# Optimization experiments

Hardware: AMD Instinct MI355X
Metric: run time of the kernel (lower is better)

The kernel has to match this reference:

```python
import jax, jax.numpy as jnp
import numpy as np

B, N, D_IN, D_OUT, R = 8, 2048, 256, 256, 4


def setup_inputs() -> dict:
    key = jax.random.key(0)
    k1, k2, k3, k4 = jax.random.split(key, 4)
    x = jax.random.normal(k1, (B, N, D_IN), dtype=jnp.float32)
    adj = jnp.zeros((1,), dtype=jnp.float32)  # unused by the module
    # relation-type matrix: 0 = no edge, 1..R = relation id
    relation = jax.random.randint(k2, (B, N, N), 0, R + 1, dtype=jnp.int32)
    weight = jax.random.normal(k3, (R, D_IN, D_OUT), dtype=jnp.float32) * 0.05
    bias = jax.random.normal(k4, (D_OUT,), dtype=jnp.float32) * 0.05
    return {"x": x, "adj": adj, "relation": relation, "weight": weight, "bias": bias}


def reference(x, adj, relation, weight, bias):
    # Binary per-relation adjacency masks: [R, B, N, N]
    rel_ids = jnp.arange(1, weight.shape[0] + 1, dtype=relation.dtype)
    masks = (relation[None] == rel_ids[:, None, None, None]).astype(x.dtype)
    # Aggregate neighbors per relation: h[r] = A_r @ x  -> [R, B, N, D_in]
    h = jnp.einsum('rbnm,bmd->rbnd', masks, x)
    # Per-relation output transform, summed over relations: [B, N, D_out]
    y = jnp.einsum('rbnd,rdo->bno', h, weight)
    return y + bias
```

## Files before the change

kernel.cpp:

```cpp
#include <hip/hip_runtime.h>
#include <hip/hip_bf16.h>
#include <stdint.h>

typedef uint32_t u32;
typedef uint64_t u64;
typedef __bf16 bf16x8 __attribute__((ext_vector_type(8)));
typedef float f32x4 __attribute__((ext_vector_type(4)));
typedef u32 u32x4 __attribute__((ext_vector_type(4)));

#define NB 8
#define NN 2048
#define DIN 256
#define DOUT 256
#define NR 4
#define KTOT (NN * NR)

#define XW_BYTES   (NB * DOUT * KTOT * 2)
#define PART_BYTES (NB * NN * DOUT * 4)

__device__ __forceinline__ ushort f2bf(float f) {
  union { float f; u32 u; } c; c.f = f;
  return (ushort)((c.u + 0x7FFFu + ((c.u >> 16) & 1u)) >> 16);
}

__device__ __forceinline__ void gload_lds16(const void* g, void* l) {
  __builtin_amdgcn_global_load_lds(
      (const __attribute__((address_space(1))) u32*)g,
      (__attribute__((address_space(3))) u32*)l, 16, 0, 0);
}

__global__ void k0_wT(const float* __restrict__ w, ushort* __restrict__ wT) {
  int i = blockIdx.x * 256 + threadIdx.x;
  int o = i & 255, d = (i >> 8) & 255, r = i >> 16;
  wT[(r * DOUT + o) * DIN + d] = f2bf(w[i]);
}

__global__ __launch_bounds__(512) void k1_xw(const float* __restrict__ x,
                                             const ushort* __restrict__ wT,
                                             ushort* __restrict__ xwT) {
  __shared__ char smem[65536];
  ushort* As = (ushort*)smem;
  ushort* Bs = (ushort*)(smem + 4096);
  const int t = threadIdx.x, l = t & 63, w = t >> 6;
  const int r = w >> 1, oh = w & 1;
  const int blk = blockIdx.x;
  const int b = blk >> 6, rest = blk & 63, mc = rest >> 1, ot = rest & 1;

  f32x4 acc[4][4] = {};
  const int arow = t >> 3, adc = (t & 7) << 2;
  const float* xg = x + ((size_t)(b * NN + mc * 64 + arow) * DIN + adc);

  for (int s = 0; s < 8; ++s) {
    const int d0 = s * 32;
    float4 xv = *(const float4*)(xg + d0);
    ushort4 a4;
    a4.x = f2bf(xv.x); a4.y = f2bf(xv.y); a4.z = f2bf(xv.z); a4.w = f2bf(xv.w);
    *(ushort4*)(As + arow * 32 + adc) = a4;
#pragma unroll
    for (int i = 0; i < 4; ++i) {
      int off = i * 4096 + t * 8;
      int rr = off >> 12, rem = off & 4095, o = rem >> 5, dd = rem & 31;
      const ushort* src = wT + ((size_t)(rr * DOUT + ot * 128 + o) * DIN + d0 + dd);
      gload_lds16(src, Bs + off);
    }
    __syncthreads();
    bf16x8 af[4];
#pragma unroll
    for (int fm = 0; fm < 4; ++fm)
      af[fm] = *(const bf16x8*)(As + (fm * 16 + (l & 15)) * 32 + (l >> 4) * 8);
#pragma unroll
    for (int fo = 0; fo < 4; ++fo) {
      bf16x8 bf = *(const bf16x8*)(Bs + (size_t)(r * 128 + oh * 64 + fo * 16 + (l & 15)) * 32 + (l >> 4) * 8);
#pragma unroll
      for (int fm = 0; fm < 4; ++fm)
        acc[fm][fo] = __builtin_amdgcn_mfma_f32_16x16x32_bf16(af[fm], bf, acc[fm][fo], 0, 0, 0);
    }
    __syncthreads();
  }
  ushort* Cs = (ushort*)smem;
#pragma unroll
  for (int fm = 0; fm < 4; ++fm)
#pragma unroll
    for (int fo = 0; fo < 4; ++fo)
#pragma unroll
      for (int j = 0; j < 4; ++j) {
        int o_loc = oh * 64 + fo * 16 + (l & 15);
        int ml = fm * 16 + (l >> 4) * 4 + j;
        Cs[o_loc * 256 + ml * 4 + r] = f2bf(acc[fm][fo][j]);
      }
  __syncthreads();
#pragma unroll
  for (int i = 0; i < 8; ++i) {
    int el = (i * 512 + t) * 8;
    int o_loc = el >> 8, kp = el & 255;
    *(uint4*)(xwT + (size_t)(b * DOUT + ot * 128 + o_loc) * KTOT + mc * 256 + kp) =
        *(const uint4*)(Cs + el);
  }
}

__global__ __launch_bounds__(256, 2) void k2_main(const int* __restrict__ rel,
                                                  const ushort* __restrict__ xwT,
                                                  float* __restrict__ out,
                                                  float* __restrict__ part) {
  __shared__ char smem[81920];
  const int t = threadIdx.x, l = t & 63, w = t >> 6;
  const int wr = w >> 1, wc = w & 1;
  const int logical = (blockIdx.x & 7) * 64 + (blockIdx.x >> 3);
  const int b = logical >> 6;
  const int nt = (logical >> 2) & 15;
  const int ks = (logical >> 1) & 1;
  const int ot = logical & 1;

  f32x4 acc[4][4] = {};
  const int arow = t >> 1, half = t & 1;
  const int* relg = rel + ((size_t)(b * NN + nt * 128 + arow) * NN + ks * 1024 + half * 8);
  const ushort* xwb = xwT + (size_t)(b * DOUT + ot * 128) * KTOT + ks * 4096;

  char* const Ab0 = smem;
  char* const Ab1 = smem + 16384;
  char* const Bb0 = smem + 32768;
  char* const Bb1 = smem + 49152;
  char* const Bb2 = smem + 65536;

  const int brow = t >> 3;
  const int kd = (((t & 7) ^ ((t >> 3) & 7)) << 3);
  const int aswz = (arow & 7) << 4;
  const int fr = l & 15, fq = l >> 4;
  const int rswz = (fr & 7) << 4;

  int4 rsA0, rsB0, rsA1, rsB1;

#define STAGE_B(S, BBASE)                                                      \
  {                                                                            \
    _Pragma("unroll") for (int i = 0; i < 4; ++i)                              \
      gload_lds16(xwb + (size_t)(brow + 32 * i) * KTOT + (S) * 64 + kd,        \
                  (BBASE) + i * 4096 + t * 16);                                \
  }

#define RELLOAD(S, RA, RB)                                                     \
  RA = *(const int4*)(relg + (S) * 16);                                        \
  RB = *(const int4*)(relg + (S) * 16 + 4);

#define EXPAND_A(ABASE, V0, V1)                                                \
  {                                                                            \
    char* rowp = (ABASE) + arow * 128;                                         \
    int vv[8] = {V0.x, V0.y, V0.z, V0.w, V1.x, V1.y, V1.z, V1.w};              \
    _Pragma("unroll") for (int p = 0; p < 4; ++p) {                            \
      int va = vv[2 * p], vb = vv[2 * p + 1];                                  \
      u32 sa = ((u32)(va - 1) & 3u) * 16u;                                     \
      u32 sb = ((u32)(vb - 1) & 3u) * 16u;                                     \
      u64 ha = va ? (0x3F80ull << sa) : 0ull;                                  \
      u64 hb = vb ? (0x3F80ull << sb) : 0ull;                                  \
      u32x4 e = {(u32)ha, (u32)(ha >> 32), (u32)hb, (u32)(hb >> 32)};          \
      *(u32x4*)(rowp + ((half * 64 + p * 16) ^ aswz)) = e;                     \
    }                                                                          \
  }

#define BARV6()                                                                \
  asm volatile("s_waitcnt vmcnt(6) lgkmcnt(0)" ::: "memory");                  \
  __builtin_amdgcn_s_barrier();                                                \
  __builtin_amdgcn_sched_barrier(0);

#define BARV0()                                                                \
  asm volatile("s_waitcnt vmcnt(0) lgkmcnt(0)" ::: "memory");                  \
  __builtin_amdgcn_s_barrier();                                                \
  __builtin_amdgcn_sched_barrier(0);

#define MFMA_STEP(AC, BC)                                                      \
  __builtin_amdgcn_s_setprio(1);                                               \
  _Pragma("unroll") for (int kk = 0; kk < 2; ++kk) {                           \
    bf16x8 af[4], bfv[4];                                                      \
    const int colb = (kk * 64 + fq * 16) ^ rswz;                               \
    _Pragma("unroll") for (int fm = 0; fm < 4; ++fm)                           \
      af[fm] = *(const bf16x8*)((AC) + (wr * 64 + fm * 16 + fr) * 128 + colb); \
    _Pragma("unroll") for (int fo = 0; fo < 4; ++fo)                           \
      bfv[fo] = *(const bf16x8*)((BC) + (wc * 64 + fo * 16 + fr) * 128 + colb);\
    _Pragma("unroll") for (int fm = 0; fm < 4; ++fm)                           \
      _Pragma("unroll") for (int fo = 0; fo < 4; ++fo)                         \
        acc[fm][fo] = __builtin_amdgcn_mfma_f32_16x16x32_bf16(                 \
            af[fm], bfv[fo], acc[fm][fo], 0, 0, 0);                            \
  }                                                                            \
  __builtin_amdgcn_s_setprio(0);

#define BODY(S, ACUR, BCUR, ANXT, RLA, RLB, RCA, RCB, BSTG)                    \
  {                                                                            \
    STAGE_B((S) + 2, BSTG);                                                    \
    RELLOAD((S) + 2, RLA, RLB);                                                \
    MFMA_STEP(ACUR, BCUR);                                                     \
    EXPAND_A(ANXT, RCA, RCB);                                                  \
    BARV6();                                                                   \
  }

  STAGE_B(0, Bb0);
  RELLOAD(0, rsA0, rsB0);
  STAGE_B(1, Bb1);
  RELLOAD(1, rsA1, rsB1);
  EXPAND_A(Ab0, rsA0, rsB0);
  BARV6();

  for (int s = 0; s < 60; s += 6) {
    BODY(s + 0, Ab0, Bb0, Ab1, rsA0, rsB0, rsA1, rsB1, Bb2);
    BODY(s + 1, Ab1, Bb1, Ab0, rsA1, rsB1, rsA0, rsB0, Bb0);
    BODY(s + 2, Ab0, Bb2, Ab1, rsA0, rsB0, rsA1, rsB1, Bb1);
    BODY(s + 3, Ab1, Bb0, Ab0, rsA1, rsB1, rsA0, rsB0, Bb2);
    BODY(s + 4, Ab0, Bb1, Ab1, rsA0, rsB0, rsA1, rsB1, Bb0);
    BODY(s + 5, Ab1, Bb2, Ab0, rsA1, rsB1, rsA0, rsB0, Bb1);
  }
  BODY(60, Ab0, Bb0, Ab1, rsA0, rsB0, rsA1, rsB1, Bb2);
  BODY(61, Ab1, Bb1, Ab0, rsA1, rsB1, rsA0, rsB0, Bb0);
  {
    MFMA_STEP(Ab0, Bb2);
    EXPAND_A(Ab1, rsA1, rsB1);
    BARV0();
  }
  {
    MFMA_STEP(Ab1, Bb0);
  }

  float* dst = ks ? part : out;
#pragma unroll
  for (int fm = 0; fm < 4; ++fm)
#pragma unroll
    for (int fo = 0; fo < 4; ++fo) {
      int n = nt * 128 + wr * 64 + fm * 16 + fq * 4;
      int o = ot * 128 + wc * 64 + fo * 16 + fr;
#pragma unroll
      for (int j = 0; j < 4; ++j)
        dst[(size_t)(b * NN + n + j) * DOUT + o] = acc[fm][fo][j];
    }
#undef BODY
#undef MFMA_STEP
#undef BARV6
#undef BARV0
#undef EXPAND_A
#undef RELLOAD
#undef STAGE_B
}

__global__ void k3_add(float* __restrict__ out, const float* __restrict__ part,
                       const float* __restrict__ bias) {
  int i = blockIdx.x * 256 + threadIdx.x;
  float4 o = ((const float4*)out)[i];
  float4 p = ((const float4*)part)[i];
  float4 bv = ((const float4*)bias)[i & 63];
  float4 rr;
  rr.x = o.x + p.x + bv.x;
  rr.y = o.y + p.y + bv.y;
  rr.z = o.z + p.z + bv.z;
  rr.w = o.w + p.w + bv.w;
  ((float4*)out)[i] = rr;
}

extern "C" void kernel_launch(void* const* d_in, const int* in_sizes, int n_in,
                              void* d_out, int out_size, void* d_ws, size_t ws_size,
                              hipStream_t stream) {
  const float* x = (const float*)d_in[0];
  const int* rel = (const int*)d_in[2];
  const float* wgt = (const float*)d_in[3];
  const float* bias = (const float*)d_in[4];
  float* out = (float*)d_out;
  char* ws = (char*)d_ws;

  ushort* xwT = (ushort*)ws;
  float* part = (float*)(ws + XW_BYTES);
  ushort* wT = (ushort*)(ws + XW_BYTES + PART_BYTES);

  k0_wT<<<1024, 256, 0, stream>>>(wgt, wT);
  k1_xw<<<512, 512, 0, stream>>>(x, wT, xwT);
  k2_main<<<512, 256, 0, stream>>>(rel, xwT, out, part);
  k3_add<<<4096, 256, 0, stream>>>(out, part, bias);
}
```

Before: 118.0 us.

## Use 256x256 tiles with 4-way split-K and bf16 partials in main GEMM

Replaces the 128x128-tile, 2-way split-K main kernel with a 512-thread, 256x256-tile kernel that covers all output columns at once, so each relation row is read and expanded only once. K is split four ways, and the partials are stored as bf16 and summed with bias in a new reduction kernel. This cuts the redundant relation-matrix traffic and the LDS expansion work, at the cost of 128KB of LDS, more accumulator registers, bf16 rounding of the partial sums, and a workspace-size check that falls back to the old path.

```diff
diff --git a/kernel.cpp b/kernel.cpp
--- a/kernel.cpp
+++ b/kernel.cpp
@@ -17,10 +17,16 @@
 
 #define XW_BYTES   (NB * DOUT * KTOT * 2)
 #define PART_BYTES (NB * NN * DOUT * 4)
+#define WT_BYTES   (NR * DIN * DOUT * 2)
+#define PART_ELEMS (NB * NN * DOUT)
 
 __device__ __forceinline__ ushort f2bf(float f) {
   union { float f; u32 u; } c; c.f = f;
   return (ushort)((c.u + 0x7FFFu + ((c.u >> 16) & 1u)) >> 16);
+}
+
+__device__ __forceinline__ float bf2f(ushort u) {
+  union { u32 i; float f; } c; c.i = ((u32)u) << 16; return c.f;
 }
 
 __device__ __forceinline__ void gload_lds16(const void* g, void* l) {
@@ -98,43 +104,41 @@
   }
 }
 
-__global__ __launch_bounds__(256, 2) void k2_main(const int* __restrict__ rel,
-                                                  const ushort* __restrict__ xwT,
-                                                  float* __restrict__ out,
-                                                  float* __restrict__ part) {
-  __shared__ char smem[81920];
+__global__ __launch_bounds__(512, 2) void k2_v2(const int* __restrict__ rel,
+                                                const ushort* __restrict__ xwT,
+                                                ushort* __restrict__ partb) {
+  __shared__ char smem[131072];
   const int t = threadIdx.x, l = t & 63, w = t >> 6;
-  const int wr = w >> 1, wc = w & 1;
-  const int logical = (blockIdx.x & 7) * 64 + (blockIdx.x >> 3);
-  const int b = logical >> 6;
-  const int nt = (logical >> 2) & 15;
-  const int ks = (logical >> 1) & 1;
-  const int ot = logical & 1;
-
-  f32x4 acc[4][4] = {};
+  const int wm = w >> 2, wn = w & 3;
+  const int logical = (blockIdx.x & 7) * 32 + (blockIdx.x >> 3);
+  const int b = logical >> 5;
+  const int nt = (logical >> 2) & 7;
+  const int ks = logical & 3;
+
+  f32x4 acc[8][4] = {};
+  const int fr = l & 15, fq = l >> 4;
+  const int rswz = (fr & 7) << 4;
+
+  char* const Ab0 = smem;
+  char* const Ab1 = smem + 32768;
+  char* const Bb0 = smem + 65536;
+  char* const Bb1 = smem + 98304;
+
   const int arow = t >> 1, half = t & 1;
-  const int* relg = rel + ((size_t)(b * NN + nt * 128 + arow) * NN + ks * 1024 + half * 8);
-  const ushort* xwb = xwT + (size_t)(b * DOUT + ot * 128) * KTOT + ks * 4096;
-
-  char* const Ab0 = smem;
-  char* const Ab1 = smem + 16384;
-  char* const Bb0 = smem + 32768;
-  char* const Bb1 = smem + 49152;
-  char* const Bb2 = smem + 65536;
+  const int aswz = (arow & 7) << 4;
+  const int* relg = rel + ((size_t)(b * NN + nt * 256 + arow)) * NN + ks * 512 + half * 8;
 
   const int brow = t >> 3;
   const int kd = (((t & 7) ^ ((t >> 3) & 7)) << 3);
-  const int aswz = (arow & 7) << 4;
-  const int fr = l & 15, fq = l >> 4;
-  const int rswz = (fr & 7) << 4;
-
-  int4 rsA0, rsB0, rsA1, rsB1;
-
-#define STAGE_B(S, BBASE)                                                      \
+  const ushort* xwb = xwT + (size_t)b * DOUT * KTOT + ks * 2048;
+
+  int4 rs0a, rs0b, rs1a, rs1b;
+
+#define GLD_ALL(S, BB)                                                         \
   {                                                                            \
     _Pragma("unroll") for (int i = 0; i < 4; ++i)                              \
-      gload_lds16(xwb + (size_t)(brow + 32 * i) * KTOT + (S) * 64 + kd,        \
-                  (BBASE) + i * 4096 + t * 16);                                \
+      gload_lds16(xwb + (size_t)(brow + 64 * i) * KTOT + (S) * 64 + kd,        \
+                  (BB) + i * 8192 + t * 16);                                   \
   }
 
 #define RELLOAD(S, RA, RB)                                                     \
@@ -156,16 +160,171 @@
     }                                                                          \
   }
 
+#define RDB(BV, BB, KK)                                                        \
+  _Pragma("unroll") for (int fo = 0; fo < 4; ++fo)                             \
+    BV[fo] = *(const bf16x8*)((BB) + (wn * 64 + fo * 16 + fr) * 128 +          \
+                              (((KK) * 64 + fq * 16) ^ rswz));
+
+#define RDA(AV, AB, FM0, KK)                                                   \
+  _Pragma("unroll") for (int i = 0; i < 4; ++i)                                \
+    AV[i] = *(const bf16x8*)((AB) + (wm * 128 + ((FM0) + i) * 16 + fr) * 128 + \
+                             (((KK) * 64 + fq * 16) ^ rswz));
+
+#define MFMA4(FM0, AV, BV)                                                     \
+  __builtin_amdgcn_s_setprio(1);                                               \
+  _Pragma("unroll") for (int i = 0; i < 4; ++i)                                \
+    _Pragma("unroll") for (int fo = 0; fo < 4; ++fo)                           \
+      acc[(FM0) + i][fo] = __builtin_amdgcn_mfma_f32_16x16x32_bf16(            \
+          AV[i], BV[fo], acc[(FM0) + i][fo], 0, 0, 0);                         \
+  __builtin_amdgcn_s_setprio(0);
+
+#define ENDFENCE(VMS)                                                          \
+  asm volatile("s_waitcnt vmcnt(" VMS ") lgkmcnt(0)" ::: "memory");            \
+  __builtin_amdgcn_s_barrier();                                                \
+  __builtin_amdgcn_sched_barrier(0);
+
+#define STEP(S, P, Q, STG, REL, EXP, VMS)                                      \
+  {                                                                            \
+    bf16x8 b0[4], b1[4], aA[4], aB[4], aC[4], aD[4];                           \
+    RDB(b0, Bb##P, 0);                                                         \
+    RDA(aA, Ab##P, 0, 0);                                                      \
+    if (STG) { GLD_ALL((S) + 1, Bb##Q); }                                      \
+    __builtin_amdgcn_sched_barrier(0);                                         \
+    if (REL) { RELLOAD((S) + 2, rs##P##a, rs##P##b); }                         \
+    RDA(aB, Ab##P, 4, 0);                                                      \
+    MFMA4(0, aA, b0);                                                          \
+    RDA(aC, Ab##P, 0, 1);                                                      \
+    if (EXP) { EXPAND_A(Ab##Q, rs##Q##a, rs##Q##b); }                          \
+    MFMA4(4, aB, b0);                                                          \
+    RDB(b1, Bb##P, 1);                                                         \
+    RDA(aD, Ab##P, 4, 1);                                                      \
+    MFMA4(0, aC, b1);                                                          \
+    MFMA4(4, aD, b1);                                                          \
+    ENDFENCE(VMS);                                                             \
+  }
+
+  GLD_ALL(0, Bb0);
+  __builtin_amdgcn_sched_barrier(0);
+  RELLOAD(0, rs0a, rs0b);
+  RELLOAD(1, rs1a, rs1b);
+  EXPAND_A(Ab0, rs0a, rs0b);
+  ENDFENCE("4");
+
+  for (int s = 0; s < 30; s += 2) {
+    STEP(s, 0, 1, 1, 1, 1, "2");
+    STEP(s + 1, 1, 0, 1, 1, 1, "2");
+  }
+  STEP(30, 0, 1, 1, 0, 1, "0");
+  {
+    bf16x8 b0[4], b1[4], aA[4], aB[4], aC[4], aD[4];
+    RDB(b0, Bb1, 0);
+    RDA(aA, Ab1, 0, 0);
+    RDA(aB, Ab1, 4, 0);
+    MFMA4(0, aA, b0);
+    RDA(aC, Ab1, 0, 1);
+    MFMA4(4, aB, b0);
+    RDB(b1, Bb1, 1);
+    RDA(aD, Ab1, 4, 1);
+    MFMA4(0, aC, b1);
+    MFMA4(4, aD, b1);
+  }
+
+  ushort* dst = partb + (size_t)ks * PART_ELEMS;
+#pragma unroll
+  for (int fm = 0; fm < 8; ++fm)
+#pragma unroll
+    for (int fo = 0; fo < 4; ++fo) {
+      int n = nt * 256 + wm * 128 + fm * 16 + fq * 4;
+      int o = wn * 64 + fo * 16 + fr;
+#pragma unroll
+      for (int j = 0; j < 4; ++j)
+        dst[(size_t)(b * NN + n + j) * DOUT + o] = f2bf(acc[fm][fo][j]);
+    }
+#undef STEP
+#undef ENDFENCE
+#undef MFMA4
+#undef RDA
+#undef RDB
+#undef EXPAND_A
+#undef RELLOAD
+#undef GLD_ALL
+}
+
+__global__ void k3_sum(float* __restrict__ out, const ushort* __restrict__ partb,
+                       const float* __restrict__ bias) {
+  int i = blockIdx.x * 256 + threadIdx.x;
+  float4 s = ((const float4*)bias)[i & 63];
+#pragma unroll
+  for (int p = 0; p < 4; ++p) {
+    ushort4 v = ((const ushort4*)(partb + (size_t)p * PART_ELEMS))[i];
+    s.x += bf2f(v.x); s.y += bf2f(v.y); s.z += bf2f(v.z); s.w += bf2f(v.w);
+  }
+  ((float4*)out)[i] = s;
+}
+
+__global__ __launch_bounds__(256, 2) void k2_r4(const int* __restrict__ rel,
+                                                const ushort* __restrict__ xwT,
+                                                float* __restrict__ out,
+                                                float* __restrict__ part) {
+  __shared__ char smem[81920];
+  const int t = threadIdx.x, l = t & 63, w = t >> 6;
+  const int wr = w >> 1, wc = w & 1;
+  const int logical = (blockIdx.x & 7) * 64 + (blockIdx.x >> 3);
+  const int b = logical >> 6;
+  const int nt = (logical >> 2) & 15;
+  const int ks = (logical >> 1) & 1;
+  const int ot = logical & 1;
+
+  f32x4 acc[4][4] = {};
+  const int arow = t >> 1, half = t & 1;
+  const int* relg = rel + ((size_t)(b * NN + nt * 128 + arow) * NN + ks * 1024 + half * 8);
+  const ushort* xwb = xwT + (size_t)(b * DOUT + ot * 128) * KTOT + ks * 4096;
+
+  char* const Ab0 = smem;
+  char* const Ab1 = smem + 16384;
+  char* const Bb0 = smem + 32768;
+  char* const Bb1 = smem + 49152;
+  char* const Bb2 = smem + 65536;
+
+  const int brow = t >> 3;
+  const int kd = (((t & 7) ^ ((t >> 3) & 7)) << 3);
+  const int aswz = (arow & 7) << 4;
+  const int fr = l & 15, fq = l >> 4;
+  const int rswz = (fr & 7) << 4;
+
+  int4 rsA0, rsB0, rsA1, rsB1;
+
+#define STAGE_B(S, BBASE)                                                      \
+  {                                                                            \
+    _Pragma("unroll") for (int i = 0; i < 4; ++i)                              \
+      gload_lds16(xwb + (size_t)(brow + 32 * i) * KTOT + (S) * 64 + kd,        \
+                  (BBASE) + i * 4096 + t * 16);                                \
+  }
+#define RELLOAD(S, RA, RB)                                                     \
+  RA = *(const int4*)(relg + (S) * 16);                                        \
+  RB = *(const int4*)(relg + (S) * 16 + 4);
+#define EXPAND_A(ABASE, V0, V1)                                                \
+  {                                                                            \
+    char* rowp = (ABASE) + arow * 128;                                         \
+    int vv[8] = {V0.x, V0.y, V0.z, V0.w, V1.x, V1.y, V1.z, V1.w};              \
+    _Pragma("unroll") for (int p = 0; p < 4; ++p) {                            \
+      int va = vv[2 * p], vb = vv[2 * p + 1];                                  \
+      u32 sa = ((u32)(va - 1) & 3u) * 16u;                                     \
+      u32 sb = ((u32)(vb - 1) & 3u) * 16u;                                     \
+      u64 ha = va ? (0x3F80ull << sa) : 0ull;                                  \
+      u64 hb = vb ? (0x3F80ull << sb) : 0ull;                                  \
+      u32x4 e = {(u32)ha, (u32)(ha >> 32), (u32)hb, (u32)(hb >> 32)};          \
+      *(u32x4*)(rowp + ((half * 64 + p * 16) ^ aswz)) = e;                     \
+    }                                                                          \
+  }
 #define BARV6()                                                                \
   asm volatile("s_waitcnt vmcnt(6) lgkmcnt(0)" ::: "memory");                  \
   __builtin_amdgcn_s_barrier();                                                \
   __builtin_amdgcn_sched_barrier(0);
-
 #define BARV0()                                                                \
   asm volatile("s_waitcnt vmcnt(0) lgkmcnt(0)" ::: "memory");                  \
   __builtin_amdgcn_s_barrier();                                                \
   __builtin_amdgcn_sched_barrier(0);
-
 #define MFMA_STEP(AC, BC)                                                      \
   __builtin_amdgcn_s_setprio(1);                                               \
   _Pragma("unroll") for (int kk = 0; kk < 2; ++kk) {                           \
@@ -181,7 +340,6 @@
             af[fm], bfv[fo], acc[fm][fo], 0, 0, 0);                            \
   }                                                                            \
   __builtin_amdgcn_s_setprio(0);
-
 #define BODY(S, ACUR, BCUR, ANXT, RLA, RLB, RCA, RCB, BSTG)                    \
   {                                                                            \
     STAGE_B((S) + 2, BSTG);                                                    \
@@ -237,8 +395,8 @@
 #undef STAGE_B
 }
 
-__global__ void k3_add(float* __restrict__ out, const float* __restrict__ part,
-                       const float* __restrict__ bias) {
+__global__ void k3_r4(float* __restrict__ out, const float* __restrict__ part,
+                      const float* __restrict__ bias) {
   int i = blockIdx.x * 256 + threadIdx.x;
   float4 o = ((const float4*)out)[i];
   float4 p = ((const float4*)part)[i];
@@ -261,12 +419,23 @@
   float* out = (float*)d_out;
   char* ws = (char*)d_ws;
 
-  ushort* xwT = (ushort*)ws;
-  float* part = (float*)(ws + XW_BYTES);
-  ushort* wT = (ushort*)(ws + XW_BYTES + PART_BYTES);
-
-  k0_wT<<<1024, 256, 0, stream>>>(wgt, wT);
-  k1_xw<<<512, 512, 0, stream>>>(x, wT, xwT);
-  k2_main<<<512, 256, 0, stream>>>(rel, xwT, out, part);
-  k3_add<<<4096, 256, 0, stream>>>(out, part, bias);
-}
+  const size_t partb_bytes = (size_t)PART_ELEMS * 2 * 4;
+  const size_t need_big = (size_t)XW_BYTES + partb_bytes + WT_BYTES;
+  if (ws_size >= need_big) {
+    ushort* xwT = (ushort*)ws;
+    ushort* partb = (ushort*)(ws + XW_BYTES);
+    ushort* wT = (ushort*)(ws + XW_BYTES + partb_bytes);
+    k0_wT<<<1024, 256, 0, stream>>>(wgt, wT);
+    k1_xw<<<512, 512, 0, stream>>>(x, wT, xwT);
+    k2_v2<<<256, 512, 0, stream>>>(rel, xwT, partb);
+    k3_sum<<<4096, 256, 0, stream>>>(out, partb, bias);
+  } else {
+    ushort* xwT = (ushort*)ws;
+    float* part = (float*)(ws + XW_BYTES);
+    ushort* wT = (ushort*)(ws + XW_BYTES + PART_BYTES);
+    k0_wT<<<1024, 256, 0, stream>>>(wgt, wT);
+    k1_xw<<<512, 512, 0, stream>>>(x, wT, xwT);
+    k2_r4<<<512, 256, 0, stream>>>(rel, xwT, out, part);
+    k3_r4<<<4096, 256, 0, stream>>>(out, part, bias);
+  }
+}
```

Result: faster. 110.3 us (-6.6%).
